# Kernel tuning notes

Hardware: AMD Instinct MI355X
Metric: run time of the kernel (lower is better)

Reference implementation:

```python
import jax, jax.numpy as jnp
import numpy as np

N_FILES = 256      # number of files (segments)
LINES = 128        # lines per file
T = N_FILES * LINES  # total lines = 32768
D_ENC = 768        # CodeBERT hidden size
HID = 256          # GCN hidden_dim
SD = 128           # shared_dim
PD = 128           # private_dim
WINDOW = 2         # line-graph window
S_AM = 30.0        # AM-Softmax scale
M_AM = 0.35        # AM-Softmax margin


def _build_edges():
    # build_line_graph: connect lines within a file at offsets 1..WINDOW, both directions
    idx = np.arange(T)
    srcs, dsts = [], []
    for off in range(1, WINDOW + 1):
        m = (idx % LINES) + off < LINES  # j stays inside the same file
        i = idx[m]; j = i + off
        srcs += [i, j]; dsts += [j, i]
    return np.stack([np.concatenate(srcs), np.concatenate(dsts)]).astype(np.int32)


def setup_inputs() -> dict:
    key = jax.random.key(0)
    ks = jax.random.split(key, 18)
    std = 0.02
    inp = {
        "line_emb": jax.random.normal(ks[0], (T, D_ENC), jnp.float32),
        "W1": jax.random.normal(ks[1], (D_ENC, HID), jnp.float32) * std,
        "b1": jnp.zeros((HID,), jnp.float32),
        "W2": jax.random.normal(ks[2], (HID, HID), jnp.float32) * std,
        "b2": jnp.zeros((HID,), jnp.float32),
        "attn_w": jax.random.normal(ks[3], (HID, 1), jnp.float32) * std,
        "attn_b": jnp.zeros((1,), jnp.float32),
        "Ws": jax.random.normal(ks[4], (HID, SD), jnp.float32) * std,
        "bs": jnp.zeros((SD,), jnp.float32),
        "Wp": jax.random.normal(ks[5], (HID, PD), jnp.float32) * std,
        "bp": jnp.zeros((PD,), jnp.float32),
        "cls_w": jax.random.normal(ks[6], (SD, 2), jnp.float32) * std,
        "Wd1": jax.random.normal(ks[7], (SD, SD), jnp.float32) * std,
        "bd1": jnp.zeros((SD,), jnp.float32),
        "Wd2": jax.random.normal(ks[8], (SD, 2), jnp.float32) * std,
        "bd2": jnp.zeros((2,), jnp.float32),
        "line_ptr": jnp.arange(0, T + 1, LINES, dtype=jnp.int32),
        "edge_index": jnp.asarray(_build_edges()),
        "file_labels": jax.random.randint(ks[9], (N_FILES,), 0, 2, jnp.int32),
    }
    return inp


def _l2norm(x):
    return x / jnp.maximum(jnp.linalg.norm(x, axis=1, keepdims=True), 1e-12)


def _gcn(x, W, b, src, dst, n):
    sl = jnp.arange(n, dtype=src.dtype)
    src = jnp.concatenate([src, sl]); dst = jnp.concatenate([dst, sl])
    deg = jax.ops.segment_sum(jnp.ones_like(src, jnp.float32), dst, num_segments=n)
    norm = jax.lax.rsqrt(deg[src] * deg[dst])  # [E+n]
    h = x @ W                                   # [n, out]
    msg = h[src] * norm[:, None]
    return jax.ops.segment_sum(msg, dst, num_segments=n) + b


def reference(line_emb, W1, b1, W2, b2, attn_w, attn_b, Ws, bs, Wp, bp,
              cls_w, Wd1, bd1, Wd2, bd2, line_ptr, edge_index, file_labels):
    n = line_emb.shape[0]
    n_files = line_ptr.shape[0] - 1
    src, dst = edge_index[0], edge_index[1]

    h = jax.nn.relu(_gcn(line_emb, W1, b1, src, dst, n))
    h = _gcn(h, W2, b2, src, dst, n)               # [T, HID]

    # ragged per-file softmax attention pooling
    seg = jnp.searchsorted(line_ptr, jnp.arange(n, dtype=line_ptr.dtype), side="right") - 1
    logits = (h @ attn_w).squeeze(-1) + attn_b[0]  # [T]
    seg_max = jax.ops.segment_max(logits, seg, num_segments=n_files)
    e = jnp.exp(logits - seg_max[seg])
    denom = jax.ops.segment_sum(e, seg, num_segments=n_files)
    att_weights = e / denom[seg]
    h_file = jax.ops.segment_sum(att_weights[:, None] * h, seg, num_segments=n_files)  # [N, HID]

    # disentangle heads
    z_shared = h_file @ Ws + bs
    z_private = h_file @ Wp + bp

    # AM-Softmax classifier (labels given -> subtract margin on true class)
    cos = _l2norm(z_shared) @ (cls_w / jnp.maximum(jnp.linalg.norm(cls_w, axis=0, keepdims=True), 1e-12))
    onehot = jax.nn.one_hot(file_labels, 2, dtype=cos.dtype)
    logits_cls = S_AM * (cos - M_AM * onehot)

    # orthogonality loss
    corr = _l2norm(z_shared).T @ _l2norm(z_private)
    ortho = jnp.linalg.norm(corr)

    # domain discriminator (GRL is identity in forward)
    domain_logits = jax.nn.relu(z_shared @ Wd1 + bd1) @ Wd2 + bd2

    return (logits_cls, h_file, z_shared, z_private, att_weights, domain_logits, ortho)
```

## Files before the change

### kernel.cpp

```cpp
#include <hip/hip_runtime.h>


typedef __attribute__((ext_vector_type(8))) short bf16x8;
typedef __attribute__((ext_vector_type(4))) short bf16x4;
typedef __attribute__((ext_vector_type(4))) float f32x4;
typedef __attribute__((ext_vector_type(8))) float f32x8;

__device__ __forceinline__ unsigned short f2bf(float f) {
  union { float f; unsigned int i; } v; v.f = f;
  unsigned int r = v.i + 0x7FFFu + ((v.i >> 16) & 1u);
  return (unsigned short)(r >> 16);
}
__device__ __forceinline__ float bf2f(unsigned short u) {
  union { unsigned int i; float f; } v; v.i = ((unsigned int)u) << 16; return v.f;
}
__device__ __forceinline__ float cvt4dot(bf16x4 v, f32x4* o) {
  (*o)[0] = bf2f(((unsigned short*)&v)[0]); (*o)[1] = bf2f(((unsigned short*)&v)[1]);
  (*o)[2] = bf2f(((unsigned short*)&v)[2]); (*o)[3] = bf2f(((unsigned short*)&v)[3]);
  return 0.f;
}
__device__ __forceinline__ int degf(int p) {
  return 5 - (p < 2 ? 2 - p : 0) - (p > 125 ? p - 125 : 0);
}
__device__ __forceinline__ float wsum(float v) {
#pragma unroll
  for (int o = 1; o < 64; o <<= 1) v += __shfl_xor(v, o);
  return v;
}

__global__ void prep_weights(const float* __restrict__ W1, const float* __restrict__ W2,
                             unsigned short* __restrict__ W1t, unsigned short* __restrict__ W2t) {
  __shared__ float tile[32][33];
  int id = blockIdx.x;
  const float* src; unsigned short* dst; int R, C, bx, by;
  if (id < 192) { src = W1; dst = W1t; R = 768; C = 256; bx = (id % 8) * 32; by = (id / 8) * 32; }
  else { id -= 192; src = W2; dst = W2t; R = 256; C = 256; bx = (id % 8) * 32; by = (id / 8) * 32; }
  int tx = threadIdx.x, ty = threadIdx.y;
#pragma unroll
  for (int j = 0; j < 32; j += 8)
    tile[ty + j][tx] = src[(by + ty + j) * C + bx + tx];
  __syncthreads();
#pragma unroll
  for (int j = 0; j < 32; j += 8)
    dst[(bx + ty + j) * R + by + tx] = f2bf(tile[tx][ty + j]);
}

__global__ __launch_bounds__(1024) void mega(const float* __restrict__ A,
    const unsigned short* __restrict__ W1t, const float* __restrict__ b1,
    const unsigned short* __restrict__ W2t, const float* __restrict__ b2,
    const float* __restrict__ attn_w, const float* __restrict__ attn_b,
    const float* __restrict__ Ws, const float* __restrict__ bs,
    const float* __restrict__ Wp, const float* __restrict__ bp,
    const float* __restrict__ cls_w, const int* __restrict__ labels,
    const float* __restrict__ Wd1, const float* __restrict__ bd1,
    const float* __restrict__ Wd2, const float* __restrict__ bd2,
    float* __restrict__ out) {
  __shared__ __align__(16) char lds[131072];
  unsigned short* sA1 = (unsigned short*)lds;
  unsigned short* sB1 = (unsigned short*)(lds + 32768);
  unsigned short* H1  = (unsigned short*)lds;
  unsigned short* G1L = (unsigned short*)(lds + 65536);
  unsigned short* sB2 = (unsigned short*)lds;
  unsigned short* H2  = (unsigned short*)lds;
  unsigned short* hB  = (unsigned short*)(lds + 65536);
  __shared__ float awS[256];
  __shared__ float lgS[128];
  __shared__ float redM[64];
  __shared__ float scr[1024];
  __shared__ float hfS[256];
  __shared__ float zsS[128], znS[128];
  __shared__ float redS[16];

  const int t = threadIdx.x;
  const int wave = t >> 6, lane = t & 63;
  const int wr = wave >> 2, wc = wave & 3;
  const int file = blockIdx.x;
  const long rowA = (long)file * 128;

  if (t < 256) awS[t] = attn_w[t];

  f32x4 acc[2][4];
#pragma unroll
  for (int m = 0; m < 2; ++m)
#pragma unroll
    for (int n = 0; n < 4; ++n) acc[m][n] = (f32x4)0.0f;

  const int arow = t >> 3, acol = (t & 7) * 8;
  const int aswz = arow * 64 + (acol ^ ((arow & 7) << 3));
  f32x8 areg;
#define ISSUE_A1(kt) areg = *(const f32x8*)&A[(rowA + arow) * 768 + (kt) * 64 + acol]
#define WRITE_A1(buf) { unsigned short u[8];                                      \
    _Pragma("unroll") for (int j = 0; j < 8; ++j) u[j] = f2bf(areg[j]);           \
    *(bf16x8*)&sA1[(buf) * 8192 + aswz] = *(bf16x8*)u; }
#define ISSUE_B1(kt, buf) _Pragma("unroll") for (int it = 0; it < 2; ++it) {      \
    int flat = (it * 1024 + t) * 8;                                               \
    int n = flat >> 6, k = flat & 63;                                             \
    const unsigned short* g = W1t + n * 768 + (kt) * 64 + (k ^ ((n & 7) << 3));   \
    __builtin_amdgcn_global_load_lds(                                             \
        (const __attribute__((address_space(1))) unsigned int*)g,                 \
        (__attribute__((address_space(3))) unsigned int*)                         \
            &sB1[(buf) * 16384 + (it * 16 + wave) * 512], 16, 0, 0); }

  ISSUE_A1(0); ISSUE_B1(0, 0); WRITE_A1(0);
  __syncthreads();
  for (int kt = 0; kt < 12; ++kt) {
    const int cur = kt & 1, nxt = cur ^ 1;
    if (kt + 1 < 12) { ISSUE_A1(kt + 1); ISSUE_B1(kt + 1, nxt); }
#pragma unroll
    for (int kk = 0; kk < 2; ++kk) {
      const int kb = kk * 32 + (lane >> 4) * 8;
      bf16x8 af[2], bfr[4];
#pragma unroll
      for (int m = 0; m < 2; ++m) {
        int r = wr * 32 + m * 16 + (lane & 15);
        af[m] = *(const bf16x8*)&sA1[cur * 8192 + r * 64 + (kb ^ ((r & 7) << 3))];
      }
#pragma unroll
      for (int n = 0; n < 4; ++n) {
        int r = wc * 64 + n * 16 + (lane & 15);
        bfr[n] = *(const bf16x8*)&sB1[cur * 16384 + r * 64 + (kb ^ ((r & 7) << 3))];
      }
#pragma unroll
      for (int m = 0; m < 2; ++m)
#pragma unroll
        for (int n = 0; n < 4; ++n)
          acc[m][n] = __builtin_amdgcn_mfma_f32_16x16x32_bf16(af[m], bfr[n], acc[m][n], 0, 0, 0);
    }
    if (kt + 1 < 12) WRITE_A1(nxt);
    __syncthreads();
  }
#pragma unroll
  for (int m = 0; m < 2; ++m)
#pragma unroll
    for (int n = 0; n < 4; ++n) {
      int r = wr * 32 + m * 16 + (lane >> 4) * 4;
      int c = wc * 64 + n * 16 + (lane & 15);
#pragma unroll
      for (int j = 0; j < 4; ++j) H1[(r + j) * 256 + c] = f2bf(acc[m][n][j]);
    }
  __syncthreads();
#pragma unroll
  for (int it = 0; it < 8; ++it) {
    int g = it * 1024 + t;
    int l = g >> 6, c0 = (g & 63) * 4;
    int dl = degf(l);
    f32x4 s = (f32x4)0.0f;
#pragma unroll
    for (int o = -2; o <= 2; ++o) {
      int q = l + o;
      if (q < 0 || q > 127) continue;
      float w = __frsqrt_rn((float)(dl * degf(q)));
      bf16x4 hv4 = *(const bf16x4*)&H1[q * 256 + c0];
      f32x4 hv; cvt4dot(hv4, &hv);
      s += w * hv;
    }
    f32x4 b = *(const f32x4*)&b1[c0];
    unsigned short o4[4];
#pragma unroll
    for (int j = 0; j < 4; ++j) o4[j] = f2bf(fmaxf(s[j] + b[j], 0.f));
    *(bf16x4*)&G1L[l * 256 + (c0 ^ ((l & 7) << 3))] = *(bf16x4*)o4;
  }
  __syncthreads();

#pragma unroll
  for (int m = 0; m < 2; ++m)
#pragma unroll
    for (int n = 0; n < 4; ++n) acc[m][n] = (f32x4)0.0f;
#define ISSUE_B2(kt, buf) _Pragma("unroll") for (int it = 0; it < 2; ++it) {      \
    int flat = (it * 1024 + t) * 8;                                               \
    int n = flat >> 6, k = flat & 63;                                             \
    const unsigned short* g = W2t + n * 256 + (kt) * 64 + (k ^ ((n & 7) << 3));   \
    __builtin_amdgcn_global_load_lds(                                             \
        (const __attribute__((address_space(1))) unsigned int*)g,                 \
        (__attribute__((address_space(3))) unsigned int*)                         \
            &sB2[(buf) * 16384 + (it * 16 + wave) * 512], 16, 0, 0); }

  ISSUE_B2(0, 0);
  __syncthreads();
  for (int kt = 0; kt < 4; ++kt) {
    const int cur = kt & 1, nxt = cur ^ 1;
    if (kt + 1 < 4) ISSUE_B2(kt + 1, nxt);
#pragma unroll
    for (int kk = 0; kk < 2; ++kk) {
      const int kb = kk * 32 + (lane >> 4) * 8;
      bf16x8 af[2], bfr[4];
#pragma unroll
      for (int m = 0; m < 2; ++m) {
        int r = wr * 32 + m * 16 + (lane & 15);
        int col = kt * 64 + kb;
        af[m] = *(const bf16x8*)&G1L[r * 256 + (col ^ ((r & 7) << 3))];
      }
#pragma unroll
      for (int n = 0; n < 4; ++n) {
        int r = wc * 64 + n * 16 + (lane & 15);
        bfr[n] = *(const bf16x8*)&sB2[cur * 16384 + r * 64 + (kb ^ ((r & 7) << 3))];
      }
#pragma unroll
      for (int m = 0; m < 2; ++m)
#pragma unroll
        for (int n = 0; n < 4; ++n)
          acc[m][n] = __builtin_amdgcn_mfma_f32_16x16x32_bf16(af[m], bfr[n], acc[m][n], 0, 0, 0);
    }
    __syncthreads();
  }
#pragma unroll
  for (int m = 0; m < 2; ++m)
#pragma unroll
    for (int n = 0; n < 4; ++n) {
      int r = wr * 32 + m * 16 + (lane >> 4) * 4;
      int c = wc * 64 + n * 16 + (lane & 15);
#pragma unroll
      for (int j = 0; j < 4; ++j) H2[(r + j) * 256 + c] = f2bf(acc[m][n][j]);
    }
  __syncthreads();
#pragma unroll
  for (int it = 0; it < 8; ++it) {
    int g = it * 1024 + t;
    int l = g >> 6, c0 = (g & 63) * 4;
    int dl = degf(l);
    f32x4 s = (f32x4)0.0f;
#pragma unroll
    for (int o = -2; o <= 2; ++o) {
      int q = l + o;
      if (q < 0 || q > 127) continue;
      float w = __frsqrt_rn((float)(dl * degf(q)));
      bf16x4 hv4 = *(const bf16x4*)&H2[q * 256 + c0];
      f32x4 hv; cvt4dot(hv4, &hv);
      s += w * hv;
    }
    f32x4 b = *(const f32x4*)&b2[c0];
    unsigned short o4[4];
#pragma unroll
    for (int j = 0; j < 4; ++j) o4[j] = f2bf(s[j] + b[j]);
    *(bf16x4*)&hB[l * 256 + c0] = *(bf16x4*)o4;
  }
  __syncthreads();

  {
    int l = t >> 3, p = t & 7;
    float part = 0.f;
#pragma unroll 4
    for (int j = 0; j < 32; ++j) {
      int c = p * 32 + ((j + 4 * p + l) & 31);
      part += bf2f(hB[l * 256 + c]) * awS[c];
    }
    part += __shfl_xor(part, 1);
    part += __shfl_xor(part, 2);
    part += __shfl_xor(part, 4);
    if (p == 0) lgS[l] = part + attn_b[0];
  }
  __syncthreads();
  if (t < 64) redM[t] = fmaxf(lgS[t], lgS[t + 64]);
  __syncthreads();
  for (int s = 32; s > 0; s >>= 1) {
    if (t < s) redM[t] = fmaxf(redM[t], redM[t + s]);
    __syncthreads();
  }
  float mx = redM[0];
  __syncthreads();
  if (t < 128) lgS[t] = expf(lgS[t] - mx);
  __syncthreads();
  if (t < 64) redM[t] = lgS[t] + lgS[t + 64];
  __syncthreads();
  for (int s = 32; s > 0; s >>= 1) {
    if (t < s) redM[t] += redM[t + s];
    __syncthreads();
  }
  float dn = redM[0];
  __syncthreads();
  if (t < 128) {
    float w = lgS[t] / dn;
    lgS[t] = w;
    out[131584 + file * 128 + t] = w;
  }
  __syncthreads();
  {
    int c = t & 255, grp = t >> 8;
    float s = 0.f;
    for (int l = grp * 32; l < grp * 32 + 32; ++l) s += lgS[l] * bf2f(hB[l * 256 + c]);
    scr[grp * 256 + c] = s;
  }
  __syncthreads();
  if (t < 256) {
    float tot = scr[t] + scr[256 + t] + scr[512 + t] + scr[768 + t];
    hfS[t] = tot;
    out[512 + file * 256 + t] = tot;
  }
  __syncthreads();

  {
    if (t < 512) {
      int g = t >> 7, j = t & 127;
      float s = 0.f;
      for (int c = g * 64; c < g * 64 + 64; ++c) s += hfS[c] * Ws[c * 128 + j];
      scr[g * 128 + j] = s;
    } else {
      int tt = t - 512, g = tt >> 7, j = tt & 127;
      float s = 0.f;
      for (int c = g * 64; c < g * 64 + 64; ++c) s += hfS[c] * Wp[c * 128 + j];
      scr[512 + g * 128 + j] = s;
    }
  }
  __syncthreads();
  {
    int j = t & 127;
    if (t < 128) {
      float zs = bs[j] + scr[j] + scr[128 + j] + scr[256 + j] + scr[384 + j];
      zsS[j] = zs;
      out[66048 + file * 128 + j] = zs;
      float s = wsum(zs * zs);
      if (lane == 0) redS[wave] = s;
    } else if (t < 256) {
      float zp = bp[j] + scr[512 + j] + scr[640 + j] + scr[768 + j] + scr[896 + j];
      out[98816 + file * 128 + j] = zp;
    }
  }
  __syncthreads();
  if (t == 0) redS[8] = fmaxf(sqrtf(redS[0] + redS[1]), 1e-12f);
  __syncthreads();
  if (t < 128) znS[t] = zsS[t] / redS[8];
  __syncthreads();
  {
    int j = t & 127;
    if (t < 512) {
      float v;
      if (t < 128)       v = znS[j] * cls_w[j * 2 + 0];
      else if (t < 256)  v = znS[j] * cls_w[j * 2 + 1];
      else if (t < 384)  { float w0 = cls_w[j * 2 + 0]; v = w0 * w0; }
      else               { float w1 = cls_w[j * 2 + 1]; v = w1 * w1; }
      float s = wsum(v);
      if (lane == 0) redS[wave] = s;
    }
  }
  __syncthreads();
  if (t == 0) {
    float d0 = redS[0] + redS[1], d1 = redS[2] + redS[3];
    float n0 = fmaxf(sqrtf(redS[4] + redS[5]), 1e-12f);
    float n1 = fmaxf(sqrtf(redS[6] + redS[7]), 1e-12f);
    int lab = labels[file];
    out[file * 2 + 0] = 30.0f * (d0 / n0 - 0.35f * (lab == 0 ? 1.f : 0.f));
    out[file * 2 + 1] = 30.0f * (d1 / n1 - 0.35f * (lab == 1 ? 1.f : 0.f));
  }
  __syncthreads();
  {
    int j = t & 127;
    if (t < 128) {
      float dd = bd1[j];
      for (int a = 0; a < 128; ++a) dd += zsS[a] * Wd1[a * 128 + j];
      dd = fmaxf(dd, 0.f);
      float s0 = wsum(dd * Wd2[j * 2 + 0]);
      if (lane == 0) redS[wave] = s0;
      float s1 = wsum(dd * Wd2[j * 2 + 1]);
      if (lane == 0) redS[4 + wave] = s1;
    }
  }
  __syncthreads();
  if (t == 0) {
    out[164352 + file * 2 + 0] = redS[0] + redS[1] + bd2[0];
    out[164352 + file * 2 + 1] = redS[4] + redS[5] + bd2[1];
  }
#undef ISSUE_A1
#undef WRITE_A1
#undef ISSUE_B1
#undef ISSUE_B2
}

__global__ __launch_bounds__(128) void znorm(const float* __restrict__ out,
                                             float* __restrict__ zsn,
                                             float* __restrict__ zpn) {
  const int f = blockIdx.x, j = threadIdx.x;
  __shared__ float red[128];
  float zs = out[66048 + f * 128 + j];
  float zp = out[98816 + f * 128 + j];
  red[j] = zs * zs; __syncthreads();
  for (int s = 64; s > 0; s >>= 1) { if (j < s) red[j] += red[j + s]; __syncthreads(); }
  float ns = sqrtf(red[0]); __syncthreads();
  zsn[f * 128 + j] = zs / fmaxf(ns, 1e-12f);
  red[j] = zp * zp; __syncthreads();
  for (int s = 64; s > 0; s >>= 1) { if (j < s) red[j] += red[j + s]; __syncthreads(); }
  float np = sqrtf(red[0]); __syncthreads();
  zpn[f * 128 + j] = zp / fmaxf(np, 1e-12f);
}

__global__ __launch_bounds__(128) void ortho_partial(const float* __restrict__ zsn,
                                                     const float* __restrict__ zpn,
                                                     float* __restrict__ partial) {
  const int a = blockIdx.x, b = threadIdx.x;
  float s = 0.f;
  for (int f = 0; f < 256; ++f) s += zsn[f * 128 + a] * zpn[f * 128 + b];
  __shared__ float red[128];
  red[b] = s * s; __syncthreads();
  for (int st = 64; st > 0; st >>= 1) { if (b < st) red[b] += red[b + st]; __syncthreads(); }
  if (b == 0) partial[a] = red[0];
}

__global__ __launch_bounds__(128) void ortho_final(const float* __restrict__ partial,
                                                   float* __restrict__ out) {
  const int t = threadIdx.x;
  __shared__ float red[128];
  red[t] = partial[t]; __syncthreads();
  for (int st = 64; st > 0; st >>= 1) { if (t < st) red[t] += red[t + st]; __syncthreads(); }
  if (t == 0) out[164864] = sqrtf(red[0]);
}

extern "C" void kernel_launch(void* const* d_in, const int* in_sizes, int n_in,
                              void* d_out, int out_size, void* d_ws, size_t ws_size,
                              hipStream_t stream) {
  const float* line_emb = (const float*)d_in[0];
  const float* W1     = (const float*)d_in[1];
  const float* b1     = (const float*)d_in[2];
  const float* W2     = (const float*)d_in[3];
  const float* b2     = (const float*)d_in[4];
  const float* attn_w = (const float*)d_in[5];
  const float* attn_b = (const float*)d_in[6];
  const float* Ws     = (const float*)d_in[7];
  const float* bs     = (const float*)d_in[8];
  const float* Wp     = (const float*)d_in[9];
  const float* bp     = (const float*)d_in[10];
  const float* cls_w  = (const float*)d_in[11];
  const float* Wd1    = (const float*)d_in[12];
  const float* bd1    = (const float*)d_in[13];
  const float* Wd2    = (const float*)d_in[14];
  const float* bd2    = (const float*)d_in[15];
  const int* labels   = (const int*)d_in[18];

  char* ws = (char*)d_ws;
  unsigned short* W1t = (unsigned short*)(ws + 0);
  unsigned short* W2t = (unsigned short*)(ws + 393216);
  float* zsn          = (float*)(ws + 524288);
  float* zpn          = (float*)(ws + 655360);
  float* partial      = (float*)(ws + 786432);
  float* out          = (float*)d_out;

  prep_weights<<<dim3(256), dim3(32, 8), 0, stream>>>(W1, W2, W1t, W2t);
  mega<<<dim3(256), dim3(1024), 0, stream>>>(line_emb, W1t, b1, W2t, b2,
                                             attn_w, attn_b, Ws, bs, Wp, bp,
                                             cls_w, labels, Wd1, bd1, Wd2, bd2, out);
  znorm<<<dim3(256), dim3(128), 0, stream>>>(out, zsn, zpn);
  ortho_partial<<<dim3(128), dim3(128), 0, stream>>>(zsn, zpn, partial);
  ortho_final<<<dim3(1), dim3(128), 0, stream>>>(partial, out);
}
```

Baseline: 74.73 us.

## Stream fp32 A tiles via async LDS loads and split Wd1 reduction

The first GEMM now loads the fp32 activation tile straight into LDS with global_load_lds, so A no longer goes through registers, and converts it to bf16 when fragments are read. It swaps __syncthreads for explicit vmcnt waits plus s_barrier, letting the next tile's loads overlap compute in both GEMM loops. The domain-discriminator Wd1 matvec is split over 512 threads with a partial-sum reduction instead of running serially on 128 threads. This doubles LDS use for A and repeats the bf16 conversion in every wave that reads the tile, and the hand-set vmcnt counts must match the number of loads issued.

```diff
diff --git a/kernel.cpp b/kernel.cpp
--- a/kernel.cpp
+++ b/kernel.cpp
@@ -13,6 +13,12 @@
 }
 __device__ __forceinline__ float bf2f(unsigned short u) {
   union { unsigned int i; float f; } v; v.i = ((unsigned int)u) << 16; return v.f;
+}
+__device__ __forceinline__ bf16x8 cvt8(f32x8 v) {
+  unsigned short u[8];
+#pragma unroll
+  for (int j = 0; j < 8; ++j) u[j] = f2bf(v[j]);
+  return *(bf16x8*)u;
 }
 __device__ __forceinline__ float cvt4dot(bf16x4 v, f32x4* o) {
   (*o)[0] = bf2f(((unsigned short*)&v)[0]); (*o)[1] = bf2f(((unsigned short*)&v)[1]);
@@ -56,8 +62,8 @@
     const float* __restrict__ Wd2, const float* __restrict__ bd2,
     float* __restrict__ out) {
   __shared__ __align__(16) char lds[131072];
-  unsigned short* sA1 = (unsigned short*)lds;
-  unsigned short* sB1 = (unsigned short*)(lds + 32768);
+  float*          sAf = (float*)lds;
+  unsigned short* sB1 = (unsigned short*)(lds + 65536);
   unsigned short* H1  = (unsigned short*)lds;
   unsigned short* G1L = (unsigned short*)(lds + 65536);
   unsigned short* sB2 = (unsigned short*)lds;
@@ -85,13 +91,14 @@
 #pragma unroll
     for (int n = 0; n < 4; ++n) acc[m][n] = (f32x4)0.0f;
 
-  const int arow = t >> 3, acol = (t & 7) * 8;
-  const int aswz = arow * 64 + (acol ^ ((arow & 7) << 3));
-  f32x8 areg;
-#define ISSUE_A1(kt) areg = *(const f32x8*)&A[(rowA + arow) * 768 + (kt) * 64 + acol]
-#define WRITE_A1(buf) { unsigned short u[8];                                      \
-    _Pragma("unroll") for (int j = 0; j < 8; ++j) u[j] = f2bf(areg[j]);           \
-    *(bf16x8*)&sA1[(buf) * 8192 + aswz] = *(bf16x8*)u; }
+#define ISSUE_A1(kt, buf) _Pragma("unroll") for (int it = 0; it < 2; ++it) {      \
+    int flat = (it * 1024 + t) * 4;           \
+    int r = flat >> 6, k = flat & 63;                                             \
+    const float* g = A + (rowA + r) * 768 + (kt) * 64 + (k ^ ((r & 7) << 3));     \
+    __builtin_amdgcn_global_load_lds(                                             \
+        (const __attribute__((address_space(1))) unsigned int*)g,                 \
+        (__attribute__((address_space(3))) unsigned int*)                         \
+            &sAf[(buf) * 8192 + (it * 16 + wave) * 256], 16, 0, 0); }
 #define ISSUE_B1(kt, buf) _Pragma("unroll") for (int it = 0; it < 2; ++it) {      \
     int flat = (it * 1024 + t) * 8;                                               \
     int n = flat >> 6, k = flat & 63;                                             \
@@ -101,11 +108,17 @@
         (__attribute__((address_space(3))) unsigned int*)                         \
             &sB1[(buf) * 16384 + (it * 16 + wave) * 512], 16, 0, 0); }
 
-  ISSUE_A1(0); ISSUE_B1(0, 0); WRITE_A1(0);
+  ISSUE_A1(0, 0); ISSUE_B1(0, 0);
   __syncthreads();
   for (int kt = 0; kt < 12; ++kt) {
     const int cur = kt & 1, nxt = cur ^ 1;
-    if (kt + 1 < 12) { ISSUE_A1(kt + 1); ISSUE_B1(kt + 1, nxt); }
+    if (kt + 1 < 12) {
+      ISSUE_A1(kt + 1, nxt); ISSUE_B1(kt + 1, nxt);
+      asm volatile("s_waitcnt vmcnt(4)" ::: "memory");
+    } else {
+      asm volatile("s_waitcnt vmcnt(0)" ::: "memory");
+    }
+    __builtin_amdgcn_sched_barrier(0);
 #pragma unroll
     for (int kk = 0; kk < 2; ++kk) {
       const int kb = kk * 32 + (lane >> 4) * 8;
@@ -113,7 +126,8 @@
 #pragma unroll
       for (int m = 0; m < 2; ++m) {
         int r = wr * 32 + m * 16 + (lane & 15);
-        af[m] = *(const bf16x8*)&sA1[cur * 8192 + r * 64 + (kb ^ ((r & 7) << 3))];
+        f32x8 a8 = *(const f32x8*)&sAf[cur * 8192 + r * 64 + (kb ^ ((r & 7) << 3))];
+        af[m] = cvt8(a8);
       }
 #pragma unroll
       for (int n = 0; n < 4; ++n) {
@@ -126,8 +140,8 @@
         for (int n = 0; n < 4; ++n)
           acc[m][n] = __builtin_amdgcn_mfma_f32_16x16x32_bf16(af[m], bfr[n], acc[m][n], 0, 0, 0);
     }
-    if (kt + 1 < 12) WRITE_A1(nxt);
-    __syncthreads();
+    __builtin_amdgcn_sched_barrier(0);
+    __builtin_amdgcn_s_barrier();
   }
 #pragma unroll
   for (int m = 0; m < 2; ++m)
@@ -179,7 +193,13 @@
   __syncthreads();
   for (int kt = 0; kt < 4; ++kt) {
     const int cur = kt & 1, nxt = cur ^ 1;
-    if (kt + 1 < 4) ISSUE_B2(kt + 1, nxt);
+    if (kt + 1 < 4) {
+      ISSUE_B2(kt + 1, nxt);
+      asm volatile("s_waitcnt vmcnt(2)" ::: "memory");
+    } else {
+      asm volatile("s_waitcnt vmcnt(0)" ::: "memory");
+    }
+    __builtin_amdgcn_sched_barrier(0);
 #pragma unroll
     for (int kk = 0; kk < 2; ++kk) {
       const int kb = kk * 32 + (lane >> 4) * 8;
@@ -201,7 +221,8 @@
         for (int n = 0; n < 4; ++n)
           acc[m][n] = __builtin_amdgcn_mfma_f32_16x16x32_bf16(af[m], bfr[n], acc[m][n], 0, 0, 0);
     }
-    __syncthreads();
+    __builtin_amdgcn_sched_barrier(0);
+    __builtin_amdgcn_s_barrier();
   }
 #pragma unroll
   for (int m = 0; m < 2; ++m)
@@ -343,11 +364,18 @@
   }
   __syncthreads();
   {
+    if (t < 512) {
+      int g = t >> 7, j = t & 127;
+      float s = 0.f;
+      for (int a = g * 32; a < g * 32 + 32; ++a) s += zsS[a] * Wd1[a * 128 + j];
+      scr[g * 128 + j] = s;
+    }
+  }
+  __syncthreads();
+  {
     int j = t & 127;
     if (t < 128) {
-      float dd = bd1[j];
-      for (int a = 0; a < 128; ++a) dd += zsS[a] * Wd1[a * 128 + j];
-      dd = fmaxf(dd, 0.f);
+      float dd = fmaxf(bd1[j] + scr[j] + scr[128 + j] + scr[256 + j] + scr[384 + j], 0.f);
       float s0 = wsum(dd * Wd2[j * 2 + 0]);
       if (lane == 0) redS[wave] = s0;
       float s1 = wsum(dd * Wd2[j * 2 + 1]);
@@ -360,7 +388,6 @@
     out[164352 + file * 2 + 1] = redS[4] + redS[5] + bd2[1];
   }
 #undef ISSUE_A1
-#undef WRITE_A1
 #undef ISSUE_B1
 #undef ISSUE_B2
 }
```

After: 73.75 us. Within noise of the previous version (-1.3%).

## Prefetch bf16 head weights into LDS asynchronously and widen head GEMVs

Applied to the files above, without the earlier changes.

The prep kernel now also converts Ws, Wp and Wd1 to bf16. The main kernel prefetches these weights into LDS with global_load_lds while attention pooling runs, so the later head GEMVs read LDS instead of strided fp32 global memory. The z_shared, z_private and discriminator GEMVs are split across all 1024 threads, with partial sums reduced through scratch, rather than only 128 or 512 threads with long serial loops. The tradeoffs are reduced precision in the head weights, extra barriers, and reuse of the LDS regions, which relies on those regions being free at that point.

```diff
diff --git a/kernel.cpp b/kernel.cpp
--- a/kernel.cpp
+++ b/kernel.cpp
@@ -29,13 +29,32 @@
 }
 
 __global__ void prep_weights(const float* __restrict__ W1, const float* __restrict__ W2,
-                             unsigned short* __restrict__ W1t, unsigned short* __restrict__ W2t) {
+                             const float* __restrict__ Ws, const float* __restrict__ Wp,
+                             const float* __restrict__ Wd1,
+                             unsigned short* __restrict__ W1t, unsigned short* __restrict__ W2t,
+                             unsigned short* __restrict__ WsbG, unsigned short* __restrict__ WpbG,
+                             unsigned short* __restrict__ Wd1bG) {
   __shared__ float tile[32][33];
   int id = blockIdx.x;
+  int tx = threadIdx.x, ty = threadIdx.y;
+  if (id >= 256) {
+    int id2 = id - 256;
+    const float* src; unsigned short* dst; int blk;
+    if (id2 < 32)      { src = Ws;  dst = WsbG;  blk = id2; }
+    else if (id2 < 64) { src = Wp;  dst = WpbG;  blk = id2 - 32; }
+    else               { src = Wd1; dst = Wd1bG; blk = id2 - 64; }
+    int tid = ty * 32 + tx;
+    int e0 = blk * 1024 + tid * 4;
+    f32x4 v = *(const f32x4*)&src[e0];
+    unsigned short o[4];
+#pragma unroll
+    for (int j = 0; j < 4; ++j) o[j] = f2bf(v[j]);
+    *(bf16x4*)&dst[e0] = *(bf16x4*)o;
+    return;
+  }
   const float* src; unsigned short* dst; int R, C, bx, by;
   if (id < 192) { src = W1; dst = W1t; R = 768; C = 256; bx = (id % 8) * 32; by = (id / 8) * 32; }
   else { id -= 192; src = W2; dst = W2t; R = 256; C = 256; bx = (id % 8) * 32; by = (id / 8) * 32; }
-  int tx = threadIdx.x, ty = threadIdx.y;
 #pragma unroll
   for (int j = 0; j < 32; j += 8)
     tile[ty + j][tx] = src[(by + ty + j) * C + bx + tx];
@@ -49,10 +68,10 @@
     const unsigned short* __restrict__ W1t, const float* __restrict__ b1,
     const unsigned short* __restrict__ W2t, const float* __restrict__ b2,
     const float* __restrict__ attn_w, const float* __restrict__ attn_b,
-    const float* __restrict__ Ws, const float* __restrict__ bs,
-    const float* __restrict__ Wp, const float* __restrict__ bp,
+    const unsigned short* __restrict__ WsbG, const float* __restrict__ bs,
+    const unsigned short* __restrict__ WpbG, const float* __restrict__ bp,
     const float* __restrict__ cls_w, const int* __restrict__ labels,
-    const float* __restrict__ Wd1, const float* __restrict__ bd1,
+    const unsigned short* __restrict__ Wd1bG, const float* __restrict__ bd1,
     const float* __restrict__ Wd2, const float* __restrict__ bd2,
     float* __restrict__ out) {
   __shared__ __align__(16) char lds[131072];
@@ -63,6 +82,8 @@
   unsigned short* sB2 = (unsigned short*)lds;
   unsigned short* H2  = (unsigned short*)lds;
   unsigned short* hB  = (unsigned short*)(lds + 65536);
+  unsigned short* Wlo = (unsigned short*)lds;
+  unsigned short* Whi = (unsigned short*)(lds + 65536);
   __shared__ float awS[256];
   __shared__ float lgS[128];
   __shared__ float redM[64];
@@ -235,6 +256,13 @@
     *(bf16x4*)&hB[l * 256 + c0] = *(bf16x4*)o4;
   }
   __syncthreads();
+#define ISSUE_WB(srcG, dstL, rounds) _Pragma("unroll") for (int it = 0; it < (rounds); ++it) { \
+    const unsigned short* g = (srcG) + (it * 1024 + t) * 8;                        \
+    __builtin_amdgcn_global_load_lds(                                              \
+        (const __attribute__((address_space(1))) unsigned int*)g,                  \
+        (__attribute__((address_space(3))) unsigned int*)                          \
+            &(dstL)[(it * 16 + wave) * 512], 16, 0, 0); }
+  ISSUE_WB(WsbG, Wlo, 4);
 
   {
     int l = t >> 3, p = t & 7;
@@ -288,37 +316,44 @@
   }
   __syncthreads();
 
-  {
-    if (t < 512) {
-      int g = t >> 7, j = t & 127;
-      float s = 0.f;
-      for (int c = g * 64; c < g * 64 + 64; ++c) s += hfS[c] * Ws[c * 128 + j];
-      scr[g * 128 + j] = s;
-    } else {
-      int tt = t - 512, g = tt >> 7, j = tt & 127;
-      float s = 0.f;
-      for (int c = g * 64; c < g * 64 + 64; ++c) s += hfS[c] * Wp[c * 128 + j];
-      scr[512 + g * 128 + j] = s;
-    }
-  }
-  __syncthreads();
-  {
-    int j = t & 127;
-    if (t < 128) {
-      float zs = bs[j] + scr[j] + scr[128 + j] + scr[256 + j] + scr[384 + j];
-      zsS[j] = zs;
-      out[66048 + file * 128 + j] = zs;
-      float s = wsum(zs * zs);
-      if (lane == 0) redS[wave] = s;
-    } else if (t < 256) {
-      float zp = bp[j] + scr[512 + j] + scr[640 + j] + scr[768 + j] + scr[896 + j];
-      out[98816 + file * 128 + j] = zp;
-    }
+  ISSUE_WB(WpbG, Whi, 4);
+  {
+    int g = t >> 7, j = t & 127;
+    float s = 0.f;
+#pragma unroll 8
+    for (int c = g * 32; c < g * 32 + 32; ++c) s += hfS[c] * bf2f(Wlo[c * 128 + j]);
+    scr[g * 128 + j] = s;
+  }
+  __syncthreads();
+  ISSUE_WB(Wd1bG, Wlo, 2);
+  if (t < 128) {
+    float zs = bs[t];
+#pragma unroll
+    for (int g = 0; g < 8; ++g) zs += scr[g * 128 + t];
+    zsS[t] = zs;
+    out[66048 + file * 128 + t] = zs;
+    float s = wsum(zs * zs);
+    if (lane == 0) redS[wave] = s;
   }
   __syncthreads();
   if (t == 0) redS[8] = fmaxf(sqrtf(redS[0] + redS[1]), 1e-12f);
-  __syncthreads();
-  if (t < 128) znS[t] = zsS[t] / redS[8];
+  {
+    int g = t >> 7, j = t & 127;
+    float s = 0.f;
+#pragma unroll 8
+    for (int c = g * 32; c < g * 32 + 32; ++c) s += hfS[c] * bf2f(Whi[c * 128 + j]);
+    scr[g * 128 + j] = s;
+  }
+  __syncthreads();
+  if (t < 128) {
+    znS[t] = zsS[t] / redS[8];
+  } else if (t < 256) {
+    int j = t - 128;
+    float zp = bp[j];
+#pragma unroll
+    for (int g = 0; g < 8; ++g) zp += scr[g * 128 + j];
+    out[98816 + file * 128 + j] = zp;
+  }
   __syncthreads();
   {
     int j = t & 127;
@@ -343,16 +378,22 @@
   }
   __syncthreads();
   {
-    int j = t & 127;
-    if (t < 128) {
-      float dd = bd1[j];
-      for (int a = 0; a < 128; ++a) dd += zsS[a] * Wd1[a * 128 + j];
-      dd = fmaxf(dd, 0.f);
-      float s0 = wsum(dd * Wd2[j * 2 + 0]);
-      if (lane == 0) redS[wave] = s0;
-      float s1 = wsum(dd * Wd2[j * 2 + 1]);
-      if (lane == 0) redS[4 + wave] = s1;
-    }
+    int g = t >> 7, j = t & 127;
+    float s = 0.f;
+#pragma unroll 8
+    for (int a = g * 16; a < g * 16 + 16; ++a) s += zsS[a] * bf2f(Wlo[a * 128 + j]);
+    scr[g * 128 + j] = s;
+  }
+  __syncthreads();
+  if (t < 128) {
+    float dd = bd1[t];
+#pragma unroll
+    for (int g = 0; g < 8; ++g) dd += scr[g * 128 + t];
+    dd = fmaxf(dd, 0.f);
+    float s0 = wsum(dd * Wd2[t * 2 + 0]);
+    if (lane == 0) redS[wave] = s0;
+    float s1 = wsum(dd * Wd2[t * 2 + 1]);
+    if (lane == 0) redS[4 + wave] = s1;
   }
   __syncthreads();
   if (t == 0) {
@@ -363,6 +404,7 @@
 #undef WRITE_A1
 #undef ISSUE_B1
 #undef ISSUE_B2
+#undef ISSUE_WB
 }
 
 __global__ __launch_bounds__(128) void znorm(const float* __restrict__ out,
@@ -425,17 +467,21 @@
   const int* labels   = (const int*)d_in[18];
 
   char* ws = (char*)d_ws;
-  unsigned short* W1t = (unsigned short*)(ws + 0);
-  unsigned short* W2t = (unsigned short*)(ws + 393216);
-  float* zsn          = (float*)(ws + 524288);
-  float* zpn          = (float*)(ws + 655360);
-  float* partial      = (float*)(ws + 786432);
-  float* out          = (float*)d_out;
-
-  prep_weights<<<dim3(256), dim3(32, 8), 0, stream>>>(W1, W2, W1t, W2t);
+  unsigned short* W1t  = (unsigned short*)(ws + 0);
+  unsigned short* W2t  = (unsigned short*)(ws + 393216);
+  float* zsn           = (float*)(ws + 524288);
+  float* zpn           = (float*)(ws + 655360);
+  float* partial       = (float*)(ws + 786432);
+  unsigned short* WsbG = (unsigned short*)(ws + 1048576);
+  unsigned short* WpbG = (unsigned short*)(ws + 1114112);
+  unsigned short* Wd1bG= (unsigned short*)(ws + 1179648);
+  float* out           = (float*)d_out;
+
+  prep_weights<<<dim3(336), dim3(32, 8), 0, stream>>>(W1, W2, Ws, Wp, Wd1,
+                                                      W1t, W2t, WsbG, WpbG, Wd1bG);
   mega<<<dim3(256), dim3(1024), 0, stream>>>(line_emb, W1t, b1, W2t, b2,
-                                             attn_w, attn_b, Ws, bs, Wp, bp,
-                                             cls_w, labels, Wd1, bd1, Wd2, bd2, out);
+                                             attn_w, attn_b, WsbG, bs, WpbG, bp,
+                                             cls_w, labels, Wd1bG, bd1, Wd2, bd2, out);
   znorm<<<dim3(256), dim3(128), 0, stream>>>(out, zsn, zpn);
   ortho_partial<<<dim3(128), dim3(128), 0, stream>>>(zsn, zpn, partial);
   ortho_final<<<dim3(1), dim3(128), 0, stream>>>(partial, out);
```

Result: faster. 73.18 us (-2.1%).
